# Performance work log

Hardware: AMD Instinct MI355X
Metric: run time of the kernel (lower is better)

## Reference

```python
import jax, jax.numpy as jnp
import numpy as np

B, F, R, L, P = 16384, 64, 1024, 4, 128  # batch, features, rules, max conditions, interaction pairs


def setup_inputs() -> dict:
    key = jax.random.key(0)
    ks = jax.random.split(key, 8)
    x = jax.random.normal(ks[0], (B, F), dtype=jnp.float32)
    attention_weights = jax.random.uniform(ks[1], (F,), dtype=jnp.float32, minval=0.5, maxval=1.5)
    premise_params = jnp.ones((R,), dtype=jnp.float32)
    rule_threshs = jax.random.normal(ks[2], (R, L), dtype=jnp.float32)
    # signs are +/-1 (split direction of each XGBoost condition)
    rule_signs = jnp.where(jax.random.randint(ks[3], (R, L), 0, 2) == 1, 1.0, -1.0).astype(jnp.float32)
    rule_masks = (jax.random.uniform(ks[4], (R, L)) < 0.9).astype(jnp.float32)
    rule_masks = rule_masks.at[:, 0].set(1.0)
    consequent_params = jax.random.normal(ks[5], (R, 1 + F + F + P), dtype=jnp.float32) * 0.01
    rule_feat_idxs = jax.random.randint(ks[6], (R, L), 0, F)
    interaction_pairs = jax.random.randint(ks[7], (P, 2), 0, F)
    return {
        "x": x,
        "attention_weights": attention_weights,
        "premise_params": premise_params,
        "rule_threshs": rule_threshs,
        "rule_signs": rule_signs,
        "rule_masks": rule_masks,
        "consequent_params": consequent_params,
        "rule_feat_idxs": rule_feat_idxs,
        "interaction_pairs": interaction_pairs,
    }


def reference(x, attention_weights, premise_params, rule_threshs, rule_signs,
              rule_masks, consequent_params, rule_feat_idxs, interaction_pairs):
    # attention scaling
    x_att = x * attention_weights  # [B, F]

    # --- fuzzify_and_infer ---
    sel = x_att[:, rule_feat_idxs]  # gather -> [B, R, L]
    z = premise_params[None, :, None] * (sel - rule_threshs[None]) * rule_signs[None]
    mf = jax.nn.sigmoid(z)
    masked_mf = mf * rule_masks[None] + (1.0 - rule_masks[None])  # inactive conds -> 1
    firing = jnp.prod(masked_mf, axis=2)  # [B, R]
    w = firing / (jnp.sum(firing, axis=1, keepdims=True) + 1e-8)  # normalized firing

    # --- TSK polynomials (order=2 with interactions): [x, x^2, xi*xj, 1] ---
    inter = x_att[:, interaction_pairs[:, 0]] * x_att[:, interaction_pairs[:, 1]]  # [B, P]
    ones = jnp.ones((x.shape[0], 1), dtype=x.dtype)
    p = jnp.concatenate([x_att, x_att * x_att, inter, ones], axis=1)  # [B, 1+2F+P]

    # weighted consequent sum: y_b = sum_r w_br * (p_b . theta_r)
    y = jnp.einsum('br,bi,ri->b', w, p, consequent_params)
    return y
```

## Files before the change

### kernel.cpp

```cpp
#include <hip/hip_runtime.h>

typedef short short8 __attribute__((ext_vector_type(8)));
typedef float f32x4 __attribute__((ext_vector_type(4)));

#define KP 288

#define OFF_CP   0ULL
#define OFF_A2   589824ULL
#define OFF_C2   606208ULL
#define OFF_IX   622592ULL
#define OFF_PAIR 626688ULL
#define OFF_NUM  626944ULL
#define OFF_DEN  692480ULL

#define XS 65

__device__ __forceinline__ unsigned short f2bf(float f) {
  unsigned u = __float_as_uint(f);
  return (unsigned short)((u + 0x7FFFu + ((u >> 16) & 1u)) >> 16);
}

__global__ __launch_bounds__(256) void prep_kernel(
    const float* __restrict__ pp, const float* __restrict__ th,
    const float* __restrict__ sg, const float* __restrict__ mk,
    const float* __restrict__ cp, const int* __restrict__ fidx,
    const int* __restrict__ pairs, unsigned char* __restrict__ ws)
{
  unsigned short* cp_out = (unsigned short*)(ws + OFF_CP);
  float* a2o = (float*)(ws + OFF_A2);
  float* c2o = (float*)(ws + OFF_C2);
  unsigned* ixo = (unsigned*)(ws + OFF_IX);
  unsigned short* pro = (unsigned short*)(ws + OFF_PAIR);
  int bid = blockIdx.x, t = threadIdx.x;

  if (bid < 288) {
    int e = bid * 1024 + t * 4;
#pragma unroll
    for (int q = 0; q < 4; ++q, ++e) {
      int r = e / KP, c = e - r * KP;
      cp_out[e] = f2bf(c < 257 ? cp[r * 257 + c] : 0.f);
    }
  } else if (bid < 292) {
    int r = (bid - 288) * 256 + t;
    float p = pp[r];
    unsigned pk = 0;
#pragma unroll
    for (int l = 0; l < 4; ++l) {
      float m = mk[r * 4 + l], s = sg[r * 4 + l], tt = th[r * 4 + l];
      float A, C;
      if (m != 0.f) { A = -1.44269504f * p * s; C = 1.44269504f * p * s * tt; }
      else          { A = 0.f;                  C = -126.f; }
      a2o[r * 4 + l] = A; c2o[r * 4 + l] = C;
      pk |= ((unsigned)fidx[r * 4 + l] & 0xFFu) << (8 * l);
    }
    ixo[r] = pk;
  } else if (bid == 292) {
    if (t < 128)
      pro[t] = (unsigned short)((pairs[2 * t] & 0xFF) | ((pairs[2 * t + 1] & 0xFF) << 8));
  } else {
    float* dst = (float*)(ws + (bid == 293 ? OFF_NUM : OFF_DEN));
#pragma unroll
    for (int q = 0; q < 64; ++q) dst[q * 256 + t] = 0.f;
  }
}

__global__ __launch_bounds__(256, 3) void main_kernel(
    const unsigned char* __restrict__ ws,
    const float* __restrict__ x, const float* __restrict__ att,
    float* __restrict__ numg, float* __restrict__ deng)
{
  __shared__ float xa[64 * XS];
  __shared__ short lCP[256 * 32];
  __shared__ short lP[64 * 32];
  __shared__ unsigned short lPair[128];

  const unsigned short* CP = (const unsigned short*)(ws + OFF_CP);
  const float4* A2p = (const float4*)(ws + OFF_A2);
  const float4* C2p = (const float4*)(ws + OFF_C2);
  const unsigned* IX = (const unsigned*)(ws + OFF_IX);
  const unsigned short* PRW = (const unsigned short*)(ws + OFF_PAIR);

  int t = threadIdx.x, l = t & 63, w = t >> 6;
  int g = l >> 4, lr = l & 15;
  int b0 = blockIdx.x * 64, r0 = blockIdx.y * 256;

  if (t < 128) lPair[t] = PRW[t];
  {
#pragma unroll
    for (int i = 0; i < 4; ++i) {
      int idx = t + i * 256, row = idx >> 4, c4 = idx & 15;
      float4 a4 = ((const float4*)att)[c4];
      float4 v = ((const float4*)(x + (size_t)(b0 + row) * 64))[c4];
      float* dst = &xa[row * XS + c4 * 4];
      dst[0] = v.x * a4.x; dst[1] = v.y * a4.y;
      dst[2] = v.z * a4.z; dst[3] = v.w * a4.w;
    }
  }
  __syncthreads();

  f32x4 acc[4][4];
#pragma unroll
  for (int mi = 0; mi < 4; ++mi)
#pragma unroll
    for (int ni = 0; ni < 4; ++ni)
      acc[mi][ni] = (f32x4){0.f, 0.f, 0.f, 0.f};

  int row2 = t >> 2, q = t & 3;
  int sw2 = (row2 ^ (row2 >> 2)) & 3;
  const float* xr2 = &xa[row2 * XS];

  short8 cpr[4];
#pragma unroll
  for (int i = 0; i < 4; ++i)
    cpr[i] = *(const short8*)(CP + (size_t)(r0 + row2 + i * 64) * KP + q * 8);

  for (int ks = 0; ks < 9; ++ks) {
    int k0 = ks * 32;
    int fb = k0 + q * 8;
    short8 vp;
    if (ks < 2) {
#pragma unroll
      for (int j = 0; j < 8; ++j) vp[j] = f2bf(xr2[fb + j]);
    } else if (ks < 4) {
#pragma unroll
      for (int j = 0; j < 8; ++j) { float u = xr2[fb - 64 + j]; vp[j] = f2bf(u * u); }
    } else if (ks < 8) {
      const unsigned* pw = (const unsigned*)&lPair[fb - 128];
#pragma unroll
      for (int u = 0; u < 4; ++u) {
        unsigned pk = pw[u];
        vp[2 * u]     = f2bf(xr2[pk & 255] * xr2[(pk >> 8) & 255]);
        vp[2 * u + 1] = f2bf(xr2[(pk >> 16) & 255] * xr2[pk >> 24]);
      }
    } else {
#pragma unroll
      for (int j = 0; j < 8; ++j) vp[j] = (fb + j == 256) ? (short)0x3F80 : (short)0;
    }
    __syncthreads();
#pragma unroll
    for (int i = 0; i < 4; ++i) {
      int rowc = row2 + i * 64;
      int swc = (rowc ^ (rowc >> 2)) & 3;
      *(short8*)&lCP[rowc * 32 + ((q ^ swc) * 8)] = cpr[i];
    }
    *(short8*)&lP[row2 * 32 + ((q ^ sw2) * 8)] = vp;
    if (ks < 8) {
#pragma unroll
      for (int i = 0; i < 4; ++i)
        cpr[i] = *(const short8*)(CP + (size_t)(r0 + row2 + i * 64) * KP + k0 + 32 + q * 8);
    }
    __syncthreads();
    short8 bF[4];
#pragma unroll
    for (int ni = 0; ni < 4; ++ni) {
      int row = ni * 16 + lr;
      int s = (row ^ (row >> 2)) & 3;
      bF[ni] = *(const short8*)&lP[row * 32 + ((g ^ s) * 8)];
    }
#pragma unroll
    for (int mi = 0; mi < 4; ++mi) {
      int row = w * 64 + mi * 16 + lr;
      int s = (row ^ (row >> 2)) & 3;
      short8 aF = *(const short8*)&lCP[row * 32 + ((g ^ s) * 8)];
#pragma unroll
      for (int ni = 0; ni < 4; ++ni)
        acc[mi][ni] = __builtin_amdgcn_mfma_f32_16x16x32_bf16(aF, bF[ni], acc[mi][ni], 0, 0, 0);
    }
  }

  float num[4] = {0.f, 0.f, 0.f, 0.f}, den[4] = {0.f, 0.f, 0.f, 0.f};
#pragma unroll
  for (int mi = 0; mi < 4; ++mi) {
#pragma unroll
    for (int j = 0; j < 4; ++j) {
      int rule = r0 + w * 64 + mi * 16 + (g << 2) + j;
      float4 A2 = A2p[rule], C2 = C2p[rule];
      unsigned pk = IX[rule];
      int f0 = pk & 255, f1 = (pk >> 8) & 255, f2 = (pk >> 16) & 255, f3 = pk >> 24;
#pragma unroll
      for (int ni = 0; ni < 4; ++ni) {
        const float* xr = &xa[(ni * 16 + lr) * XS];
        float D = 1.f;
        float e0 = exp2f(fmaf(A2.x, xr[f0], C2.x)); D = fmaf(D, e0, D);
        float e1 = exp2f(fmaf(A2.y, xr[f1], C2.y)); D = fmaf(D, e1, D);
        float e2 = exp2f(fmaf(A2.z, xr[f2], C2.z)); D = fmaf(D, e2, D);
        float e3 = exp2f(fmaf(A2.w, xr[f3], C2.w)); D = fmaf(D, e3, D);
        float fir = __builtin_amdgcn_rcpf(D);
        num[ni] = fmaf(fir, acc[mi][ni][j], num[ni]);
        den[ni] += fir;
      }
    }
  }

#pragma unroll
  for (int ni = 0; ni < 4; ++ni) {
    float n = num[ni], d = den[ni];
    n += __shfl_xor(n, 16, 64); n += __shfl_xor(n, 32, 64);
    d += __shfl_xor(d, 16, 64); d += __shfl_xor(d, 32, 64);
    num[ni] = n; den[ni] = d;
  }
  float nv = 0.f, dv = 0.f;
#pragma unroll
  for (int ni = 0; ni < 4; ++ni)
    if (g == ni) { nv = num[ni]; dv = den[ni]; }
  atomicAdd(&numg[b0 + (g << 4) + lr], nv);
  atomicAdd(&deng[b0 + (g << 4) + lr], dv);
}

__global__ __launch_bounds__(256) void fin_kernel(
    const float* __restrict__ numg, const float* __restrict__ deng,
    float* __restrict__ y)
{
  int i = blockIdx.x * 256 + threadIdx.x;
  y[i] = numg[i] / (deng[i] + 1e-8f);
}

extern "C" void kernel_launch(void* const* d_in, const int* in_sizes, int n_in,
                              void* d_out, int out_size, void* d_ws, size_t ws_size,
                              hipStream_t stream) {
  (void)in_sizes; (void)n_in; (void)out_size; (void)ws_size;
  const float* x    = (const float*)d_in[0];
  const float* att  = (const float*)d_in[1];
  const float* pp   = (const float*)d_in[2];
  const float* th   = (const float*)d_in[3];
  const float* sg   = (const float*)d_in[4];
  const float* mk   = (const float*)d_in[5];
  const float* cp   = (const float*)d_in[6];
  const int* fidx   = (const int*)d_in[7];
  const int* pairs  = (const int*)d_in[8];
  unsigned char* ws = (unsigned char*)d_ws;
  float* numg = (float*)(ws + OFF_NUM);
  float* deng = (float*)(ws + OFF_DEN);

  prep_kernel<<<295, 256, 0, stream>>>(pp, th, sg, mk, cp, fidx, pairs, ws);
  main_kernel<<<dim3(256, 4), 256, 0, stream>>>(ws, x, att, numg, deng);
  fin_kernel<<<64, 256, 0, stream>>>(numg, deng, (float*)d_out);
}
```

Measured before the change: 104.5 us.

## Fold constant-term consequent into epilogue bias and double-buffer CP prefetch

The constant polynomial term (consequent column 256) is no longer handled as a ninth, mostly zero-padded K-slice of the bf16 MFMA GEMM. It is stored as a separate fp32 per-rule bias and added to the accumulator in the epilogue. This cuts K from 288 to 256, removing one k-step with its two barriers and its MFMAs, and lets the prep kernel drop the per-element divide. The CP register prefetch is also double-buffered two steps ahead with unroll 2, at the cost of extra registers under a 3-waves occupancy bound.

Result: slower. 107.5 us (+2.9%).

```diff
diff --git a/kernel.cpp b/kernel.cpp
--- a/kernel.cpp
+++ b/kernel.cpp
@@ -3,15 +3,15 @@
 typedef short short8 __attribute__((ext_vector_type(8)));
 typedef float f32x4 __attribute__((ext_vector_type(4)));
 
-#define KP 288
 
 #define OFF_CP   0ULL
-#define OFF_A2   589824ULL
-#define OFF_C2   606208ULL
-#define OFF_IX   622592ULL
-#define OFF_PAIR 626688ULL
-#define OFF_NUM  626944ULL
-#define OFF_DEN  692480ULL
+#define OFF_CB   524288ULL
+#define OFF_A2   528384ULL
+#define OFF_C2   544768ULL
+#define OFF_IX   561152ULL
+#define OFF_PAIR 565248ULL
+#define OFF_NUM  565504ULL
+#define OFF_DEN  631040ULL
 
 #define XS 65
 
@@ -27,21 +27,21 @@
     const int* __restrict__ pairs, unsigned char* __restrict__ ws)
 {
   unsigned short* cp_out = (unsigned short*)(ws + OFF_CP);
+  float* cbo = (float*)(ws + OFF_CB);
   float* a2o = (float*)(ws + OFF_A2);
   float* c2o = (float*)(ws + OFF_C2);
   unsigned* ixo = (unsigned*)(ws + OFF_IX);
   unsigned short* pro = (unsigned short*)(ws + OFF_PAIR);
   int bid = blockIdx.x, t = threadIdx.x;
 
-  if (bid < 288) {
+  if (bid < 256) {
     int e = bid * 1024 + t * 4;
-#pragma unroll
-    for (int q = 0; q < 4; ++q, ++e) {
-      int r = e / KP, c = e - r * KP;
-      cp_out[e] = f2bf(c < 257 ? cp[r * 257 + c] : 0.f);
-    }
-  } else if (bid < 292) {
-    int r = (bid - 288) * 256 + t;
+    int r = e >> 8, c = e & 255;
+    const float* src = cp + (size_t)r * 257 + c;
+#pragma unroll
+    for (int q = 0; q < 4; ++q) cp_out[e + q] = f2bf(src[q]);
+  } else if (bid < 260) {
+    int r = (bid - 256) * 256 + t;
     float p = pp[r];
     unsigned pk = 0;
 #pragma unroll
@@ -54,11 +54,12 @@
       pk |= ((unsigned)fidx[r * 4 + l] & 0xFFu) << (8 * l);
     }
     ixo[r] = pk;
-  } else if (bid == 292) {
+    cbo[r] = cp[(size_t)r * 257 + 256];
+  } else if (bid == 260) {
     if (t < 128)
       pro[t] = (unsigned short)((pairs[2 * t] & 0xFF) | ((pairs[2 * t + 1] & 0xFF) << 8));
   } else {
-    float* dst = (float*)(ws + (bid == 293 ? OFF_NUM : OFF_DEN));
+    float* dst = (float*)(ws + (bid == 261 ? OFF_NUM : OFF_DEN));
 #pragma unroll
     for (int q = 0; q < 64; ++q) dst[q * 256 + t] = 0.f;
   }
@@ -75,6 +76,7 @@
   __shared__ unsigned short lPair[128];
 
   const unsigned short* CP = (const unsigned short*)(ws + OFF_CP);
+  const float* CB = (const float*)(ws + OFF_CB);
   const float4* A2p = (const float4*)(ws + OFF_A2);
   const float4* C2p = (const float4*)(ws + OFF_C2);
   const unsigned* IX = (const unsigned*)(ws + OFF_IX);
@@ -108,13 +110,17 @@
   int row2 = t >> 2, q = t & 3;
   int sw2 = (row2 ^ (row2 >> 2)) & 3;
   const float* xr2 = &xa[row2 * XS];
-
-  short8 cpr[4];
-#pragma unroll
-  for (int i = 0; i < 4; ++i)
-    cpr[i] = *(const short8*)(CP + (size_t)(r0 + row2 + i * 64) * KP + q * 8);
-
-  for (int ks = 0; ks < 9; ++ks) {
+  const unsigned short* cpbase = CP + (size_t)(r0 + row2) * 256 + q * 8;
+
+  short8 cpr[2][4];
+#pragma unroll
+  for (int i = 0; i < 4; ++i) {
+    cpr[0][i] = *(const short8*)(cpbase + (size_t)i * 64 * 256);
+    cpr[1][i] = *(const short8*)(cpbase + (size_t)i * 64 * 256 + 32);
+  }
+
+#pragma unroll 2
+  for (int ks = 0; ks < 8; ++ks) {
     int k0 = ks * 32;
     int fb = k0 + q * 8;
     short8 vp;
@@ -124,7 +130,7 @@
     } else if (ks < 4) {
 #pragma unroll
       for (int j = 0; j < 8; ++j) { float u = xr2[fb - 64 + j]; vp[j] = f2bf(u * u); }
-    } else if (ks < 8) {
+    } else {
       const unsigned* pw = (const unsigned*)&lPair[fb - 128];
 #pragma unroll
       for (int u = 0; u < 4; ++u) {
@@ -132,22 +138,19 @@
         vp[2 * u]     = f2bf(xr2[pk & 255] * xr2[(pk >> 8) & 255]);
         vp[2 * u + 1] = f2bf(xr2[(pk >> 16) & 255] * xr2[pk >> 24]);
       }
-    } else {
-#pragma unroll
-      for (int j = 0; j < 8; ++j) vp[j] = (fb + j == 256) ? (short)0x3F80 : (short)0;
     }
     __syncthreads();
 #pragma unroll
     for (int i = 0; i < 4; ++i) {
       int rowc = row2 + i * 64;
       int swc = (rowc ^ (rowc >> 2)) & 3;
-      *(short8*)&lCP[rowc * 32 + ((q ^ swc) * 8)] = cpr[i];
+      *(short8*)&lCP[rowc * 32 + ((q ^ swc) * 8)] = cpr[ks & 1][i];
     }
     *(short8*)&lP[row2 * 32 + ((q ^ sw2) * 8)] = vp;
-    if (ks < 8) {
+    if (ks < 6) {
 #pragma unroll
       for (int i = 0; i < 4; ++i)
-        cpr[i] = *(const short8*)(CP + (size_t)(r0 + row2 + i * 64) * KP + k0 + 32 + q * 8);
+        cpr[ks & 1][i] = *(const short8*)(cpbase + (size_t)i * 64 * 256 + k0 + 64);
     }
     __syncthreads();
     short8 bF[4];
@@ -176,6 +179,7 @@
       int rule = r0 + w * 64 + mi * 16 + (g << 2) + j;
       float4 A2 = A2p[rule], C2 = C2p[rule];
       unsigned pk = IX[rule];
+      float bias = CB[rule];
       int f0 = pk & 255, f1 = (pk >> 8) & 255, f2 = (pk >> 16) & 255, f3 = pk >> 24;
 #pragma unroll
       for (int ni = 0; ni < 4; ++ni) {
@@ -186,7 +190,7 @@
         float e2 = exp2f(fmaf(A2.z, xr[f2], C2.z)); D = fmaf(D, e2, D);
         float e3 = exp2f(fmaf(A2.w, xr[f3], C2.w)); D = fmaf(D, e3, D);
         float fir = __builtin_amdgcn_rcpf(D);
-        num[ni] = fmaf(fir, acc[mi][ni][j], num[ni]);
+        num[ni] = fmaf(fir, acc[mi][ni][j] + bias, num[ni]);
         den[ni] += fir;
       }
     }
@@ -232,7 +236,7 @@
   float* numg = (float*)(ws + OFF_NUM);
   float* deng = (float*)(ws + OFF_DEN);
 
-  prep_kernel<<<295, 256, 0, stream>>>(pp, th, sg, mk, cp, fidx, pairs, ws);
+  prep_kernel<<<263, 256, 0, stream>>>(pp, th, sg, mk, cp, fidx, pairs, ws);
   main_kernel<<<dim3(256, 4), 256, 0, stream>>>(ws, x, att, numg, deng);
   fin_kernel<<<64, 256, 0, stream>>>(numg, deng, (float*)d_out);
 }
```
